# Optimization experiments

Measured on AMD Instinct MI355X. Metric: run time of the kernel, lower is better.

The kernel has to match this reference:

```python
import jax, jax.numpy as jnp
import numpy as np

HEADS = 4
ALPHA = 0.2  # leaky relu negative slope


def setup_inputs() -> dict:
    key = jax.random.key(0)
    ks = jax.random.split(key, 8)
    N, Fin, Fout = 4096, 512, 256
    return {
        "h": jax.random.normal(ks[0], (N, Fin), dtype=jnp.float32),
        "adj": jax.random.randint(ks[1], (N, N), 0, 2, dtype=jnp.int32),
        "W": jax.random.normal(ks[2], (Fin, Fout), dtype=jnp.float32) * (Fin ** -0.5),
        "Wl_w": jax.random.normal(ks[3], (Fout, Fout), dtype=jnp.float32) * (Fout ** -0.5),
        "Wl_b": jax.random.normal(ks[4], (Fout,), dtype=jnp.float32) * 0.02,
        "Wqkv_w": jax.random.normal(ks[5], (3 * Fout, Fout), dtype=jnp.float32) * (Fout ** -0.5),
        "Wqkv_b": jax.random.normal(ks[6], (3 * Fout,), dtype=jnp.float32) * 0.02,
        "a": jax.random.normal(ks[7], (2 * Fout, 1), dtype=jnp.float32) * (Fout ** -0.5),
    }


def reference(h, adj, W, Wl_w, Wl_b, Wqkv_w, Wqkv_b, a):
    N = h.shape[0]
    Fout = W.shape[1]
    d = Fout // HEADS
    scale = Fout ** -0.5  # note: original scales by out_features^-0.5, not head_dim

    Wh = h @ W                      # [N, Fout]
    Wh = Wh @ Wl_w.T + Wl_b         # to_linear

    qkv = Wh @ Wqkv_w.T + Wqkv_b    # [N, 3*Fout]
    q, k, v = jnp.split(qkv, 3, axis=-1)
    to_heads = lambda t: t.reshape(N, HEADS, d).transpose(1, 0, 2)  # [H, N, d]
    q, k, v = to_heads(q), to_heads(k), to_heads(v)

    dots = jax.nn.softmax(jnp.einsum('hid,hjd->hij', q, k) * scale, axis=-1)  # [H,N,N]
    Wh0 = jnp.einsum('hij,hjd->hid', dots, v)            # [H, N, d]
    Wh0 = Wh0.transpose(1, 0, 2).reshape(N, Fout)        # i (h d)
    Wh0 = jax.nn.softmax(Wh0, axis=-1)

    # GAT score decomposed: e_ij = leakyrelu(Wh_i . a1 + Wh_j . a2)
    a1 = a[:Fout, 0]
    a2 = a[Fout:, 0]
    e = jax.nn.leaky_relu((Wh @ a1)[:, None] + (Wh @ a2)[None, :], negative_slope=ALPHA)

    dsum = dots.sum(axis=0)                              # [N, N]
    neg = jnp.float32(-9e15)
    attention = jnp.where(adj > 0, e + dsum, neg)
    attention = jax.nn.softmax(attention, axis=1)
    # dropout p=0.0 / eval mode -> identity

    h_prime = attention @ Wh + Wh0
    return jax.nn.elu(h_prime)  # concat=True
```

## Files before the change

### kernel.cpp

```cpp
#include <hip/hip_runtime.h>

typedef float  f32x4 __attribute__((ext_vector_type(4)));
typedef short  s16x8 __attribute__((ext_vector_type(8)));
typedef unsigned short u16x8 __attribute__((ext_vector_type(8)));

#define NROWS 4096
#define FOUT  256
#define ALPHA_LR 0.2f
#define SCALE 0.0625f
#define NEGV  -9.0e15f

static __device__ __forceinline__ unsigned short bf16_rne(float x) {
    unsigned u = __float_as_uint(x);
    u += 0x7fffu + ((u >> 16) & 1u);
    return (unsigned short)(u >> 16);
}
static __device__ __forceinline__ float bf2f(unsigned short h) {
    return __uint_as_float(((unsigned)h) << 16);
}
static __device__ __forceinline__ float wmax16(float v) {
#pragma unroll
    for (int o = 8; o; o >>= 1) v = fmaxf(v, __shfl_xor(v, o, 16));
    return v;
}
static __device__ __forceinline__ float wsum16(float v) {
#pragma unroll
    for (int o = 8; o; o >>= 1) v += __shfl_xor(v, o, 16);
    return v;
}
static __device__ __forceinline__ float wmax32(float v) {
#pragma unroll
    for (int o = 16; o; o >>= 1) v = fmaxf(v, __shfl_xor(v, o, 32));
    return v;
}
static __device__ __forceinline__ float wsum32(float v) {
#pragma unroll
    for (int o = 16; o; o >>= 1) v += __shfl_xor(v, o, 32);
    return v;
}

template <bool BT, bool BIAS, int EPI>
__global__ __launch_bounds__(256) void gemm_f32(
    const float* __restrict__ A, const float* __restrict__ B,
    const float* __restrict__ bias, float* __restrict__ C,
    unsigned short* __restrict__ o0, unsigned short* __restrict__ o1,
    unsigned short* __restrict__ o2,
    int M, int Nn, int K)
{
    __shared__ float As[16][68];
    __shared__ float Bs[16][68];

    const int tid = threadIdx.x;
    const int bm = blockIdx.y * 64;
    const int bn = blockIdx.x * 64;
    const int tx = tid & 15;
    const int ty = tid >> 4;

    float acc[4][4];
#pragma unroll
    for (int r = 0; r < 4; ++r)
#pragma unroll
        for (int c = 0; c < 4; ++c) acc[r][c] = 0.0f;

    for (int k0 = 0; k0 < K; k0 += 16) {
        __syncthreads();
        {
            const int r = tid >> 2;
            const int c4 = (tid & 3) * 4;
            float4 a4 = *(const float4*)&A[(size_t)(bm + r) * K + k0 + c4];
            As[c4 + 0][r] = a4.x; As[c4 + 1][r] = a4.y;
            As[c4 + 2][r] = a4.z; As[c4 + 3][r] = a4.w;
        }
        if (!BT) {
            const int r = tid >> 4;
            const int c4 = (tid & 15) * 4;
            *(float4*)&Bs[r][c4] = *(const float4*)&B[(size_t)(k0 + r) * Nn + bn + c4];
        } else {
            const int r = tid >> 2;
            const int c4 = (tid & 3) * 4;
            float4 b4 = *(const float4*)&B[(size_t)(bn + r) * K + k0 + c4];
            Bs[c4 + 0][r] = b4.x; Bs[c4 + 1][r] = b4.y;
            Bs[c4 + 2][r] = b4.z; Bs[c4 + 3][r] = b4.w;
        }
        __syncthreads();
#pragma unroll
        for (int kk = 0; kk < 16; ++kk) {
            float4 a4 = *(const float4*)&As[kk][ty * 4];
            float4 b4 = *(const float4*)&Bs[kk][tx * 4];
            acc[0][0] += a4.x * b4.x; acc[0][1] += a4.x * b4.y; acc[0][2] += a4.x * b4.z; acc[0][3] += a4.x * b4.w;
            acc[1][0] += a4.y * b4.x; acc[1][1] += a4.y * b4.y; acc[1][2] += a4.y * b4.z; acc[1][3] += a4.y * b4.w;
            acc[2][0] += a4.z * b4.x; acc[2][1] += a4.z * b4.y; acc[2][2] += a4.z * b4.z; acc[2][3] += a4.z * b4.w;
            acc[3][0] += a4.w * b4.x; acc[3][1] += a4.w * b4.y; acc[3][2] += a4.w * b4.z; acc[3][3] += a4.w * b4.w;
        }
    }

    float bv[4] = {0.f, 0.f, 0.f, 0.f};
    if (BIAS) {
#pragma unroll
        for (int c = 0; c < 4; ++c) bv[c] = bias[bn + tx * 4 + c];
    }

    if (EPI == 0) {
#pragma unroll
        for (int r = 0; r < 4; ++r) {
            float4 o;
            o.x = acc[r][0] + bv[0]; o.y = acc[r][1] + bv[1];
            o.z = acc[r][2] + bv[2]; o.w = acc[r][3] + bv[3];
            *(float4*)&C[(size_t)(bm + ty * 4 + r) * Nn + bn + tx * 4] = o;
        }
    } else {
#pragma unroll
        for (int r = 0; r < 4; ++r) {
            const int row = bm + ty * 4 + r;
#pragma unroll
            for (int c = 0; c < 4; ++c) {
                const int col = bn + tx * 4 + c;
                float v = acc[r][c] + bv[c];
                if (EPI == 1) {
                    C[(size_t)row * Nn + col] = v;
                    o0[(size_t)col * NROWS + row] = bf16_rne(v);
                } else {
                    if (col < 256)      o0[(size_t)row * 256 + col] = bf16_rne(v);
                    else if (col < 512) o1[(size_t)row * 256 + (col - 256)] = bf16_rne(v);
                    else                o2[(size_t)(col - 512) * NROWS + row] = bf16_rne(v);
                }
            }
        }
    }
}

__global__ __launch_bounds__(256) void compute_p(
    const float* __restrict__ Wh, const float* __restrict__ a,
    float* __restrict__ p1, float* __restrict__ p2)
{
    const int row = blockIdx.x * 16 + (threadIdx.x >> 4);
    const int c = threadIdx.x & 15;
    float s1 = 0.f, s2 = 0.f;
    for (int f = c; f < FOUT; f += 16) {
        float w = Wh[(size_t)row * FOUT + f];
        s1 += w * a[f];
        s2 += w * a[FOUT + f];
    }
    s1 = wsum16(s1);
    s2 = wsum16(s2);
    if (c == 0) { p1[row] = s1; p2[row] = s2; }
}

__global__ __launch_bounds__(256) void stats_kernel(
    const unsigned short* __restrict__ qh_g, const unsigned short* __restrict__ kh_g,
    float* __restrict__ stats)
{
    const int tid = threadIdx.x;
    const int h = tid >> 6;
    const int ln = tid & 63;
    const int l15 = ln & 15;
    const int lhi = ln >> 4;
    const int rt = blockIdx.x >> 3;
    const int ch = blockIdx.x & 7;
    const int i0 = rt * 16;

    s16x8 qA[2];
#pragma unroll
    for (int ks = 0; ks < 2; ++ks)
        qA[ks] = *(const s16x8*)(qh_g + (size_t)(i0 + l15) * 256 + h * 64 + ks * 32 + lhi * 8);

    float m[4], z[4];
#pragma unroll
    for (int r = 0; r < 4; ++r) { m[r] = -3.0e38f; z[r] = 0.f; }

    for (int tt = 0; tt < 16; ++tt) {
        const int j0 = ch * 512 + tt * 32;
        f32x4 acc[2] = {{0.f,0.f,0.f,0.f},{0.f,0.f,0.f,0.f}};
#pragma unroll
        for (int ks = 0; ks < 2; ++ks)
#pragma unroll
            for (int nt = 0; nt < 2; ++nt) {
                s16x8 kB = *(const s16x8*)(kh_g + (size_t)(j0 + nt * 16 + l15) * 256 +
                                           h * 64 + ks * 32 + lhi * 8);
                acc[nt] = __builtin_amdgcn_mfma_f32_16x16x32_bf16(qA[ks], kB, acc[nt], 0, 0, 0);
            }
#pragma unroll
        for (int r = 0; r < 4; ++r) {
            float s0 = acc[0][r] * SCALE, s1 = acc[1][r] * SCALE;
            float mn = fmaxf(m[r], fmaxf(s0, s1));
            z[r] = z[r] * __expf(m[r] - mn) + __expf(s0 - mn) + __expf(s1 - mn);
            m[r] = mn;
        }
    }
#pragma unroll
    for (int r = 0; r < 4; ++r) {
        float mm = m[r], zz = z[r];
#pragma unroll
        for (int o = 1; o < 16; o <<= 1) {
            float mo = __shfl_xor(mm, o, 16);
            float zo = __shfl_xor(zz, o, 16);
            float mn = fmaxf(mm, mo);
            zz = zz * __expf(mm - mn) + zo * __expf(mo - mn);
            mm = mn;
        }
        if (l15 == 0) {
            size_t idx = (((size_t)(i0 + lhi * 4 + r) * 4 + h) * 8 + ch) * 2;
            stats[idx] = mm;
            stats[idx + 1] = zz;
        }
    }
}

__global__ __launch_bounds__(512, 4) void main_attn(
    const unsigned short* __restrict__ qh_g, const unsigned short* __restrict__ kh_g,
    const unsigned short* __restrict__ vth_g, const unsigned short* __restrict__ wht_g,
    const float* __restrict__ stats, const float* __restrict__ p1g,
    const float* __restrict__ p2g, const int* __restrict__ adj,
    unsigned short* __restrict__ pacc_o, unsigned short* __restrict__ wacc_o,
    float* __restrict__ ml_o)
{
    enum { KT = 0, VT = 16896, WHT = 37376, DOTS = 57856, PTIL = 62976,
           ALP = 64256, MIZ = 64320, SMEMSZ = 64832 };
    __shared__ __align__(16) char smem[SMEMSZ];

    const int tid = threadIdx.x;
    const int w = tid >> 6;
    const int h = w & 3;
    const int jg = w >> 2;
    const int ln = tid & 63;
    const int l15 = ln & 15;
    const int lhi = ln >> 4;
    const int rt = blockIdx.x >> 1;
    const int ch = blockIdx.x & 1;
    const int i0 = rt * 16;
    const int jbase = ch * 2048;
    const int srow = tid >> 5;
    const int scol = tid & 31;

    if (tid < 64) {
        int hh = tid >> 4, row = tid & 15;
        const float* sb = stats + ((size_t)(i0 + row) * 4 + hh) * 16;
        float M = -3.0e38f, Z = 0.f;
#pragma unroll
        for (int c = 0; c < 8; ++c) {
            float mc = sb[c * 2], zc = sb[c * 2 + 1];
            float mn = fmaxf(M, mc);
            Z = Z * __expf(M - mn) + zc * __expf(mc - mn);
            M = mn;
        }
        ((float*)(smem + MIZ))[(hh * 16 + row) * 2] = M;
        ((float*)(smem + MIZ))[(hh * 16 + row) * 2 + 1] = 1.0f / Z;
    }

    int laK[2], gK[2], laV[2], gV[2];
#pragma unroll
    for (int it = 0; it < 2; ++it) {
        int c = tid + it * 512;
        int kr = c >> 5, kc = c & 31;
        laK[it] = kr * 528 + kc * 16;
        gK[it] = kr * 256 + kc * 8;
        int vd = c >> 2, vc = c & 3;
        laV[it] = vd * 80 + vc * 16;
        gV[it] = vd * 4096 + vc * 8;
    }

#pragma unroll
    for (int it = 0; it < 2; ++it) {
        *(uint4*)(smem + KT + laK[it])  = *(const uint4*)(kh_g  + (size_t)jbase * 256 + gK[it]);
        *(uint4*)(smem + VT + laV[it])  = *(const uint4*)(vth_g + (size_t)jbase + gV[it]);
        *(uint4*)(smem + WHT + laV[it]) = *(const uint4*)(wht_g + (size_t)jbase + gV[it]);
    }

    s16x8 qA[2];
#pragma unroll
    for (int ks = 0; ks < 2; ++ks)
        qA[ks] = *(const s16x8*)(qh_g + (size_t)(i0 + l15) * 256 + h * 64 + ks * 32 + lhi * 8);

    __syncthreads();

    float m_f[4], iz_f[4];
#pragma unroll
    for (int r = 0; r < 4; ++r) {
        m_f[r]  = ((float*)(smem + MIZ))[(h * 16 + lhi * 4 + r) * 2];
        iz_f[r] = ((float*)(smem + MIZ))[(h * 16 + lhi * 4 + r) * 2 + 1];
    }

    int kaddr[2];
#pragma unroll
    for (int ks = 0; ks < 2; ++ks)
        kaddr[ks] = KT + (jg * 16 + l15) * 528 + h * 128 + ks * 64 + lhi * 16;
    const int daddr = DOTS + h * 1280 + l15 * 80 + lhi * 16;
    const int paddr = PTIL + l15 * 80 + lhi * 16;
    int vaddr[2], waddr[2];
#pragma unroll
    for (int nt = 0; nt < 2; ++nt) {
        int d = h * 64 + jg * 32 + nt * 16 + l15;
        vaddr[nt] = VT + d * 80 + lhi * 16;
        waddr[nt] = WHT + d * 80 + lhi * 16;
    }
    const int dwbase = DOTS + h * 1280 + jg * 32 + l15 * 2;

    f32x4 pacc[2] = {{0.f,0.f,0.f,0.f},{0.f,0.f,0.f,0.f}};
    f32x4 wacc[2] = {{0.f,0.f,0.f,0.f},{0.f,0.f,0.f,0.f}};
    float Mrun = -3.0e38f, Lrun = 0.0f;
    const float p1v = p1g[i0 + srow];

    int   adjc = adj[(size_t)(i0 + srow) * NROWS + jbase + scol];
    float p2c  = p2g[jbase + scol];

    for (int t = 0; t < 64; ++t) {
        const int jn = jbase + ((t + 1) & 63) * 32;
        uint4 kr0 = *(const uint4*)(kh_g + (size_t)jn * 256 + gK[0]);
        uint4 kr1 = *(const uint4*)(kh_g + (size_t)jn * 256 + gK[1]);

        f32x4 qk = {0.f,0.f,0.f,0.f};
        __builtin_amdgcn_s_setprio(1);
        {
            s16x8 k0 = *(const s16x8*)(smem + kaddr[0]);
            s16x8 k1 = *(const s16x8*)(smem + kaddr[1]);
            qk = __builtin_amdgcn_mfma_f32_16x16x32_bf16(qA[0], k0, qk, 0, 0, 0);
            qk = __builtin_amdgcn_mfma_f32_16x16x32_bf16(qA[1], k1, qk, 0, 0, 0);
        }
        __builtin_amdgcn_s_setprio(0);
#pragma unroll
        for (int r = 0; r < 4; ++r) {
            float d = __expf(qk[r] * SCALE - m_f[r]) * iz_f[r];
            *(unsigned short*)(smem + dwbase + (lhi * 4 + r) * 80) = bf16_rne(d);
        }
        __syncthreads();

        *(uint4*)(smem + KT + laK[0]) = kr0;
        *(uint4*)(smem + KT + laK[1]) = kr1;
        uint4 vr0 = *(const uint4*)(vth_g + (size_t)jn + gV[0]);
        uint4 vr1 = *(const uint4*)(vth_g + (size_t)jn + gV[1]);
        uint4 wr0 = *(const uint4*)(wht_g + (size_t)jn + gV[0]);
        uint4 wr1 = *(const uint4*)(wht_g + (size_t)jn + gV[1]);
        int   adjn = adj[(size_t)(i0 + srow) * NROWS + jn + scol];
        float p2n  = p2g[jn + scol];

        __builtin_amdgcn_s_setprio(1);
        {
            s16x8 dA = *(const s16x8*)(smem + daddr);
            s16x8 v0 = *(const s16x8*)(smem + vaddr[0]);
            s16x8 v1 = *(const s16x8*)(smem + vaddr[1]);
            pacc[0] = __builtin_amdgcn_mfma_f32_16x16x32_bf16(dA, v0, pacc[0], 0, 0, 0);
            pacc[1] = __builtin_amdgcn_mfma_f32_16x16x32_bf16(dA, v1, pacc[1], 0, 0, 0);
        }
        __builtin_amdgcn_s_setprio(0);

        {
            float ds = 0.f;
#pragma unroll
            for (int hh = 0; hh < 4; ++hh)
                ds += bf2f(*(const unsigned short*)(smem + DOTS + hh * 1280 + srow * 80 + scol * 2));
            float e = p1v + p2c; e = e > 0.f ? e : ALPHA_LR * e;
            float l = adjc > 0 ? e + ds : NEGV;
            float tm = wmax32(l);
            float Mn = fmaxf(Mrun, tm);
            float p = __expf(l - Mn);
            float ps = wsum32(p);
            float al = __expf(Mrun - Mn);
            Lrun = Lrun * al + ps;
            Mrun = Mn;
            if ((ln & 31) == 0) *(float*)(smem + ALP + srow * 4) = al;
            *(unsigned short*)(smem + PTIL + srow * 80 + scol * 2) = bf16_rne(p);
        }
        __syncthreads();

        *(uint4*)(smem + VT + laV[0]) = vr0;
        *(uint4*)(smem + VT + laV[1]) = vr1;

        {
            float al_r[4];
#pragma unroll
            for (int r = 0; r < 4; ++r)
                al_r[r] = *(const float*)(smem + ALP + (lhi * 4 + r) * 4);
#pragma unroll
            for (int nt = 0; nt < 2; ++nt)
#pragma unroll
                for (int r = 0; r < 4; ++r) wacc[nt][r] *= al_r[r];
            s16x8 pA = *(const s16x8*)(smem + paddr);
            s16x8 w0 = *(const s16x8*)(smem + waddr[0]);
            s16x8 w1 = *(const s16x8*)(smem + waddr[1]);
            __builtin_amdgcn_s_setprio(1);
            wacc[0] = __builtin_amdgcn_mfma_f32_16x16x32_bf16(pA, w0, wacc[0], 0, 0, 0);
            wacc[1] = __builtin_amdgcn_mfma_f32_16x16x32_bf16(pA, w1, wacc[1], 0, 0, 0);
            __builtin_amdgcn_s_setprio(0);
        }
        __syncthreads();

        *(uint4*)(smem + WHT + laV[0]) = wr0;
        *(uint4*)(smem + WHT + laV[1]) = wr1;

        adjc = adjn; p2c = p2n;
    }

    const size_t pbase = (size_t)(rt * 2 + ch) * 16 * 256;
#pragma unroll
    for (int nt = 0; nt < 2; ++nt)
#pragma unroll
        for (int r = 0; r < 4; ++r) {
            int row = lhi * 4 + r;
            int col = h * 64 + jg * 32 + nt * 16 + l15;
            pacc_o[pbase + row * 256 + col] = bf16_rne(pacc[nt][r]);
            wacc_o[pbase + row * 256 + col] = bf16_rne(wacc[nt][r]);
        }
    if ((ln & 31) == 0) {
        ml_o[((size_t)(rt * 2 + ch) * 16 + srow) * 2]     = Mrun;
        ml_o[((size_t)(rt * 2 + ch) * 16 + srow) * 2 + 1] = Lrun;
    }
}

__global__ __launch_bounds__(256) void merge_kernel(
    const unsigned short* __restrict__ pacc_b, const unsigned short* __restrict__ wacc_b,
    const float* __restrict__ ml, float* __restrict__ out)
{
    const int rt = blockIdx.x;
    const int tid = threadIdx.x;
    const int row = tid >> 4;
    const int cg = tid & 15;

    const size_t b0 = ((size_t)(rt * 2 + 0) * 16 + row) * 256 + cg * 16;
    const size_t b1 = ((size_t)(rt * 2 + 1) * 16 + row) * 256 + cg * 16;
    float M0 = ml[((size_t)(rt * 2 + 0) * 16 + row) * 2];
    float L0 = ml[((size_t)(rt * 2 + 0) * 16 + row) * 2 + 1];
    float M1 = ml[((size_t)(rt * 2 + 1) * 16 + row) * 2];
    float L1 = ml[((size_t)(rt * 2 + 1) * 16 + row) * 2 + 1];
    float M = fmaxf(M0, M1);
    float s0 = __expf(M0 - M), s1 = __expf(M1 - M);
    float invL = 1.0f / (L0 * s0 + L1 * s1);

    u16x8 pa[2][2], wa[2][2];
#pragma unroll
    for (int k = 0; k < 2; ++k) {
        pa[0][k] = *(const u16x8*)(pacc_b + b0 + k * 8);
        pa[1][k] = *(const u16x8*)(pacc_b + b1 + k * 8);
        wa[0][k] = *(const u16x8*)(wacc_b + b0 + k * 8);
        wa[1][k] = *(const u16x8*)(wacc_b + b1 + k * 8);
    }
    float p[16], wv[16];
    float mx = -3.0e38f;
#pragma unroll
    for (int k = 0; k < 16; ++k) {
        p[k] = bf2f(pa[0][k >> 3][k & 7]) + bf2f(pa[1][k >> 3][k & 7]);
        wv[k] = (bf2f(wa[0][k >> 3][k & 7]) * s0 + bf2f(wa[1][k >> 3][k & 7]) * s1) * invL;
        mx = fmaxf(mx, p[k]);
    }
    mx = wmax16(mx);
    float sm = 0.f;
#pragma unroll
    for (int k = 0; k < 16; ++k) { p[k] = __expf(p[k] - mx); sm += p[k]; }
    sm = wsum16(sm);
    float inv = 1.0f / sm;
    float* orow = out + ((size_t)(rt * 16 + row)) * 256 + cg * 16;
#pragma unroll
    for (int k4 = 0; k4 < 4; ++k4) {
        float4 o;
        float v;
        v = wv[k4*4+0] + p[k4*4+0] * inv; o.x = v > 0.f ? v : __expf(v) - 1.f;
        v = wv[k4*4+1] + p[k4*4+1] * inv; o.y = v > 0.f ? v : __expf(v) - 1.f;
        v = wv[k4*4+2] + p[k4*4+2] * inv; o.z = v > 0.f ? v : __expf(v) - 1.f;
        v = wv[k4*4+3] + p[k4*4+3] * inv; o.w = v > 0.f ? v : __expf(v) - 1.f;
        *(float4*)(orow + k4 * 4) = o;
    }
}

extern "C" void kernel_launch(void* const* d_in, const int* in_sizes, int n_in,
                              void* d_out, int out_size, void* d_ws, size_t ws_size,
                              hipStream_t stream)
{
    const float* h      = (const float*)d_in[0];
    const int*   adj    = (const int*)d_in[1];
    const float* W      = (const float*)d_in[2];
    const float* Wl_w   = (const float*)d_in[3];
    const float* Wl_b   = (const float*)d_in[4];
    const float* Wqkv_w = (const float*)d_in[5];
    const float* Wqkv_b = (const float*)d_in[6];
    const float* a      = (const float*)d_in[7];
    float* out = (float*)d_out;

    float* ws = (float*)d_ws;
    float* T   = ws;
    float* Whb = ws + (1 << 20);
    unsigned short* qh  = (unsigned short*)(ws + (2 << 20));
    unsigned short* kh  = qh + (1 << 20);
    unsigned short* vth = kh + (1 << 20);
    unsigned short* wht = vth + (1 << 20);
    float* p1b    = ws + (4 << 20);
    float* p2b    = p1b + 4096;
    float* statsb = p2b + 4096;
    float* mlb    = statsb + 262144;
    unsigned short* pacc_b = (unsigned short*)T;
    unsigned short* wacc_b = (unsigned short*)Whb;

    dim3 blk(256);
    gemm_f32<false, false, 0><<<dim3(4, 64), blk, 0, stream>>>(
        h, W, nullptr, T, nullptr, nullptr, nullptr, 4096, 256, 512);
    gemm_f32<true, true, 1><<<dim3(4, 64), blk, 0, stream>>>(
        T, Wl_w, Wl_b, Whb, wht, nullptr, nullptr, 4096, 256, 256);
    gemm_f32<true, true, 2><<<dim3(12, 64), blk, 0, stream>>>(
        Whb, Wqkv_w, Wqkv_b, nullptr, qh, kh, vth, 4096, 768, 256);
    compute_p<<<dim3(256), blk, 0, stream>>>(Whb, a, p1b, p2b);
    stats_kernel<<<dim3(2048), blk, 0, stream>>>(qh, kh, statsb);
    main_attn<<<dim3(512), dim3(512), 0, stream>>>(
        qh, kh, vth, wht, statsb, p1b, p2b, adj, pacc_b, wacc_b, mlb);
    merge_kernel<<<dim3(256), blk, 0, stream>>>(pacc_b, wacc_b, mlb, out);
}
```

Before: 289.6 us.

## Use split-bf16 MFMA GEMMs, fold W into Wl, and stream attention operands from registers

Replaces the FP32 SIMT GEMMs with MFMA GEMMs that emulate fp32 precision by splitting each operand into bf16 hi/lo parts and issuing three MFMAs per tile. The two input linear layers are algebraically combined: Wl_w·Wᵀ is computed once into a combined weight, so the large 4096-row pass runs a single GEMM instead of two. Separately, main_attn drops its K/V/Wh LDS staging and instead loads MFMA fragments straight from global memory into registers with one-step prefetch, cutting shared memory and one barrier per iteration. The trade-offs are slightly different rounding from the hi/lo split and reassociated GEMMs, plus less coalesced global fragment loads in the attention loop.

```diff
diff --git a/kernel.cpp b/kernel.cpp
--- a/kernel.cpp
+++ b/kernel.cpp
@@ -15,6 +15,9 @@
     u += 0x7fffu + ((u >> 16) & 1u);
     return (unsigned short)(u >> 16);
 }
+static __device__ __forceinline__ unsigned short bf16_trunc(float x) {
+    return (unsigned short)(__float_as_uint(x) >> 16);
+}
 static __device__ __forceinline__ float bf2f(unsigned short h) {
     return __uint_as_float(((unsigned)h) << 16);
 }
@@ -39,91 +42,117 @@
     return v;
 }
 
-template <bool BT, bool BIAS, int EPI>
-__global__ __launch_bounds__(256) void gemm_f32(
-    const float* __restrict__ A, const float* __restrict__ B,
-    const float* __restrict__ bias, float* __restrict__ C,
-    unsigned short* __restrict__ o0, unsigned short* __restrict__ o1,
-    unsigned short* __restrict__ o2,
+__global__ __launch_bounds__(256) void wprep(
+    const float* __restrict__ W, const float* __restrict__ Wq,
+    unsigned short* __restrict__ Whi, unsigned short* __restrict__ Wlo,
+    unsigned short* __restrict__ Qhi, unsigned short* __restrict__ Qlo)
+{
+    int i = blockIdx.x * 256 + threadIdx.x;
+    if (i < 131072) {
+        float v = W[i];
+        unsigned short hh = bf16_trunc(v);
+        Whi[i] = hh; Wlo[i] = bf16_rne(v - bf2f(hh));
+    }
+    if (i < 196608) {
+        float v = Wq[i];
+        unsigned short hh = bf16_trunc(v);
+        Qhi[i] = hh; Qlo[i] = bf16_rne(v - bf2f(hh));
+    }
+}
+
+template <int EPI, bool BIAS>
+__global__ __launch_bounds__(256) void gemm_mfma(
+    const float* __restrict__ A,
+    const unsigned short* __restrict__ Bhi, const unsigned short* __restrict__ Blo,
+    const float* __restrict__ bias,
+    float* __restrict__ C, unsigned short* __restrict__ o0,
+    unsigned short* __restrict__ o1, unsigned short* __restrict__ o2,
     int M, int Nn, int K)
 {
-    __shared__ float As[16][68];
-    __shared__ float Bs[16][68];
+    __shared__ unsigned short Ah[64][40];
+    __shared__ unsigned short Al[64][40];
+    __shared__ unsigned short Bh[64][40];
+    __shared__ unsigned short Bl[64][40];
 
     const int tid = threadIdx.x;
+    const int w = tid >> 6;
+    const int ln = tid & 63;
+    const int l15 = ln & 15;
+    const int lhi = ln >> 4;
     const int bm = blockIdx.y * 64;
     const int bn = blockIdx.x * 64;
-    const int tx = tid & 15;
-    const int ty = tid >> 4;
-
-    float acc[4][4];
-#pragma unroll
-    for (int r = 0; r < 4; ++r)
-#pragma unroll
-        for (int c = 0; c < 4; ++c) acc[r][c] = 0.0f;
-
-    for (int k0 = 0; k0 < K; k0 += 16) {
+    const int sm = tid >> 2;
+    const int sk = (tid & 3) * 8;
+
+    f32x4 acc[4];
+#pragma unroll
+    for (int cf = 0; cf < 4; ++cf) acc[cf] = (f32x4){0.f, 0.f, 0.f, 0.f};
+
+    const float* arow = &A[(size_t)(bm + sm) * K];
+    const unsigned short* bhrow = &Bhi[(size_t)(bn + sm) * K];
+    const unsigned short* blrow = &Blo[(size_t)(bn + sm) * K];
+
+    float4 a0r = *(const float4*)(arow + sk);
+    float4 a1r = *(const float4*)(arow + sk + 4);
+    uint4 bhr = *(const uint4*)(bhrow + sk);
+    uint4 blr = *(const uint4*)(blrow + sk);
+
+    for (int k0 = 0; k0 < K; k0 += 32) {
+        float vv[8] = {a0r.x, a0r.y, a0r.z, a0r.w, a1r.x, a1r.y, a1r.z, a1r.w};
+        unsigned hp[4], lp[4];
+#pragma unroll
+        for (int q = 0; q < 4; ++q) {
+            unsigned short h0 = bf16_trunc(vv[q * 2]);
+            unsigned short h1 = bf16_trunc(vv[q * 2 + 1]);
+            unsigned short l0 = bf16_rne(vv[q * 2] - bf2f(h0));
+            unsigned short l1 = bf16_rne(vv[q * 2 + 1] - bf2f(h1));
+            hp[q] = (unsigned)h0 | ((unsigned)h1 << 16);
+            lp[q] = (unsigned)l0 | ((unsigned)l1 << 16);
+        }
         __syncthreads();
-        {
-            const int r = tid >> 2;
-            const int c4 = (tid & 3) * 4;
-            float4 a4 = *(const float4*)&A[(size_t)(bm + r) * K + k0 + c4];
-            As[c4 + 0][r] = a4.x; As[c4 + 1][r] = a4.y;
-            As[c4 + 2][r] = a4.z; As[c4 + 3][r] = a4.w;
-        }
-        if (!BT) {
-            const int r = tid >> 4;
-            const int c4 = (tid & 15) * 4;
-            *(float4*)&Bs[r][c4] = *(const float4*)&B[(size_t)(k0 + r) * Nn + bn + c4];
-        } else {
-            const int r = tid >> 2;
-            const int c4 = (tid & 3) * 4;
-            float4 b4 = *(const float4*)&B[(size_t)(bn + r) * K + k0 + c4];
-            Bs[c4 + 0][r] = b4.x; Bs[c4 + 1][r] = b4.y;
-            Bs[c4 + 2][r] = b4.z; Bs[c4 + 3][r] = b4.w;
-        }
+        *(uint4*)&Ah[sm][sk] = make_uint4(hp[0], hp[1], hp[2], hp[3]);
+        *(uint4*)&Al[sm][sk] = make_uint4(lp[0], lp[1], lp[2], lp[3]);
+        *(uint4*)&Bh[sm][sk] = bhr;
+        *(uint4*)&Bl[sm][sk] = blr;
+        const int kn = (k0 + 32 < K) ? k0 + 32 : 0;
+        a0r = *(const float4*)(arow + kn + sk);
+        a1r = *(const float4*)(arow + kn + sk + 4);
+        bhr = *(const uint4*)(bhrow + kn + sk);
+        blr = *(const uint4*)(blrow + kn + sk);
         __syncthreads();
-#pragma unroll
-        for (int kk = 0; kk < 16; ++kk) {
-            float4 a4 = *(const float4*)&As[kk][ty * 4];
-            float4 b4 = *(const float4*)&Bs[kk][tx * 4];
-            acc[0][0] += a4.x * b4.x; acc[0][1] += a4.x * b4.y; acc[0][2] += a4.x * b4.z; acc[0][3] += a4.x * b4.w;
-            acc[1][0] += a4.y * b4.x; acc[1][1] += a4.y * b4.y; acc[1][2] += a4.y * b4.z; acc[1][3] += a4.y * b4.w;
-            acc[2][0] += a4.z * b4.x; acc[2][1] += a4.z * b4.y; acc[2][2] += a4.z * b4.z; acc[2][3] += a4.z * b4.w;
-            acc[3][0] += a4.w * b4.x; acc[3][1] += a4.w * b4.y; acc[3][2] += a4.w * b4.z; acc[3][3] += a4.w * b4.w;
-        }
-    }
-
-    float bv[4] = {0.f, 0.f, 0.f, 0.f};
-    if (BIAS) {
-#pragma unroll
-        for (int c = 0; c < 4; ++c) bv[c] = bias[bn + tx * 4 + c];
-    }
-
-    if (EPI == 0) {
+        s16x8 ah = *(const s16x8*)&Ah[w * 16 + l15][lhi * 8];
+        s16x8 al2 = *(const s16x8*)&Al[w * 16 + l15][lhi * 8];
+        __builtin_amdgcn_s_setprio(1);
+#pragma unroll
+        for (int cf = 0; cf < 4; ++cf) {
+            s16x8 bh = *(const s16x8*)&Bh[cf * 16 + l15][lhi * 8];
+            s16x8 bl = *(const s16x8*)&Bl[cf * 16 + l15][lhi * 8];
+            acc[cf] = __builtin_amdgcn_mfma_f32_16x16x32_bf16(ah, bh, acc[cf], 0, 0, 0);
+            acc[cf] = __builtin_amdgcn_mfma_f32_16x16x32_bf16(ah, bl, acc[cf], 0, 0, 0);
+            acc[cf] = __builtin_amdgcn_mfma_f32_16x16x32_bf16(al2, bh, acc[cf], 0, 0, 0);
+        }
+        __builtin_amdgcn_s_setprio(0);
+    }
+
+#pragma unroll
+    for (int cf = 0; cf < 4; ++cf) {
+        const int col = bn + cf * 16 + l15;
+        float bv = BIAS ? bias[col] : 0.0f;
 #pragma unroll
         for (int r = 0; r < 4; ++r) {
-            float4 o;
-            o.x = acc[r][0] + bv[0]; o.y = acc[r][1] + bv[1];
-            o.z = acc[r][2] + bv[2]; o.w = acc[r][3] + bv[3];
-            *(float4*)&C[(size_t)(bm + ty * 4 + r) * Nn + bn + tx * 4] = o;
-        }
-    } else {
-#pragma unroll
-        for (int r = 0; r < 4; ++r) {
-            const int row = bm + ty * 4 + r;
-#pragma unroll
-            for (int c = 0; c < 4; ++c) {
-                const int col = bn + tx * 4 + c;
-                float v = acc[r][c] + bv[c];
-                if (EPI == 1) {
-                    C[(size_t)row * Nn + col] = v;
-                    o0[(size_t)col * NROWS + row] = bf16_rne(v);
-                } else {
-                    if (col < 256)      o0[(size_t)row * 256 + col] = bf16_rne(v);
-                    else if (col < 512) o1[(size_t)row * 256 + (col - 256)] = bf16_rne(v);
-                    else                o2[(size_t)(col - 512) * NROWS + row] = bf16_rne(v);
-                }
+            const int row = bm + w * 16 + lhi * 4 + r;
+            float v = acc[cf][r] + bv;
+            if (EPI == 1) {
+                C[(size_t)row * Nn + col] = v;
+                o0[(size_t)col * NROWS + row] = bf16_rne(v);
+            } else if (EPI == 2) {
+                if (col < 256)      o0[(size_t)row * 256 + col] = bf16_rne(v);
+                else if (col < 512) o1[(size_t)row * 256 + (col - 256)] = bf16_rne(v);
+                else                o2[(size_t)(col - 512) * NROWS + row] = bf16_rne(v);
+            } else {
+                unsigned short hh = bf16_trunc(v);
+                o0[(size_t)row * Nn + col] = hh;
+                o1[(size_t)row * Nn + col] = bf16_rne(v - bf2f(hh));
             }
         }
     }
@@ -214,8 +243,7 @@
     unsigned short* __restrict__ pacc_o, unsigned short* __restrict__ wacc_o,
     float* __restrict__ ml_o)
 {
-    enum { KT = 0, VT = 16896, WHT = 37376, DOTS = 57856, PTIL = 62976,
-           ALP = 64256, MIZ = 64320, SMEMSZ = 64832 };
+    enum { DOTS = 0, PTIL = 5120, ALP = 6400, MIZ = 6464, SMEMSZ = 6976 };
     __shared__ __align__(16) char smem[SMEMSZ];
 
     const int tid = threadIdx.x;
@@ -247,25 +275,6 @@
         ((float*)(smem + MIZ))[(hh * 16 + row) * 2 + 1] = 1.0f / Z;
     }
 
-    int laK[2], gK[2], laV[2], gV[2];
-#pragma unroll
-    for (int it = 0; it < 2; ++it) {
-        int c = tid + it * 512;
-        int kr = c >> 5, kc = c & 31;
-        laK[it] = kr * 528 + kc * 16;
-        gK[it] = kr * 256 + kc * 8;
-        int vd = c >> 2, vc = c & 3;
-        laV[it] = vd * 80 + vc * 16;
-        gV[it] = vd * 4096 + vc * 8;
-    }
-
-#pragma unroll
-    for (int it = 0; it < 2; ++it) {
-        *(uint4*)(smem + KT + laK[it])  = *(const uint4*)(kh_g  + (size_t)jbase * 256 + gK[it]);
-        *(uint4*)(smem + VT + laV[it])  = *(const uint4*)(vth_g + (size_t)jbase + gV[it]);
-        *(uint4*)(smem + WHT + laV[it]) = *(const uint4*)(wht_g + (size_t)jbase + gV[it]);
-    }
-
     s16x8 qA[2];
 #pragma unroll
     for (int ks = 0; ks < 2; ++ks)
@@ -280,43 +289,38 @@
         iz_f[r] = ((float*)(smem + MIZ))[(h * 16 + lhi * 4 + r) * 2 + 1];
     }
 
-    int kaddr[2];
-#pragma unroll
-    for (int ks = 0; ks < 2; ++ks)
-        kaddr[ks] = KT + (jg * 16 + l15) * 528 + h * 128 + ks * 64 + lhi * 16;
-    const int daddr = DOTS + h * 1280 + l15 * 80 + lhi * 16;
-    const int paddr = PTIL + l15 * 80 + lhi * 16;
-    int vaddr[2], waddr[2];
-#pragma unroll
-    for (int nt = 0; nt < 2; ++nt) {
-        int d = h * 64 + jg * 32 + nt * 16 + l15;
-        vaddr[nt] = VT + d * 80 + lhi * 16;
-        waddr[nt] = WHT + d * 80 + lhi * 16;
-    }
-    const int dwbase = DOTS + h * 1280 + jg * 32 + l15 * 2;
+    const unsigned short* kp = kh_g + (size_t)(jg * 16 + l15) * 256 + h * 64 + lhi * 8;
+    const unsigned short* vp = vth_g + (size_t)(h * 64 + jg * 32 + l15) * 4096 + lhi * 8;
+    const unsigned short* wp = wht_g + (size_t)(h * 64 + jg * 32 + l15) * 4096 + lhi * 8;
+
+    s16x8 kf0 = *(const s16x8*)(kp + (size_t)jbase * 256);
+    s16x8 kf1 = *(const s16x8*)(kp + (size_t)jbase * 256 + 32);
+    s16x8 vf0 = *(const s16x8*)(vp + jbase);
+    s16x8 vf1 = *(const s16x8*)(vp + 16 * 4096 + jbase);
+    s16x8 wf0 = *(const s16x8*)(wp + jbase);
+    s16x8 wf1 = *(const s16x8*)(wp + 16 * 4096 + jbase);
+    int   adjc = adj[(size_t)(i0 + srow) * NROWS + jbase + scol];
+    float p2c  = p2g[jbase + scol];
 
     f32x4 pacc[2] = {{0.f,0.f,0.f,0.f},{0.f,0.f,0.f,0.f}};
     f32x4 wacc[2] = {{0.f,0.f,0.f,0.f},{0.f,0.f,0.f,0.f}};
     float Mrun = -3.0e38f, Lrun = 0.0f;
     const float p1v = p1g[i0 + srow];
 
-    int   adjc = adj[(size_t)(i0 + srow) * NROWS + jbase + scol];
-    float p2c  = p2g[jbase + scol];
+    const int dwbase = DOTS + h * 1280 + (jg * 16 + l15) * 2;
+    const int daddr  = DOTS + h * 1280 + l15 * 80 + lhi * 16;
+    const int paddr  = PTIL + l15 * 80 + lhi * 16;
 
     for (int t = 0; t < 64; ++t) {
         const int jn = jbase + ((t + 1) & 63) * 32;
-        uint4 kr0 = *(const uint4*)(kh_g + (size_t)jn * 256 + gK[0]);
-        uint4 kr1 = *(const uint4*)(kh_g + (size_t)jn * 256 + gK[1]);
-
-        f32x4 qk = {0.f,0.f,0.f,0.f};
+
+        f32x4 qk = {0.f, 0.f, 0.f, 0.f};
         __builtin_amdgcn_s_setprio(1);
-        {
-            s16x8 k0 = *(const s16x8*)(smem + kaddr[0]);
-            s16x8 k1 = *(const s16x8*)(smem + kaddr[1]);
-            qk = __builtin_amdgcn_mfma_f32_16x16x32_bf16(qA[0], k0, qk, 0, 0, 0);
-            qk = __builtin_amdgcn_mfma_f32_16x16x32_bf16(qA[1], k1, qk, 0, 0, 0);
-        }
+        qk = __builtin_amdgcn_mfma_f32_16x16x32_bf16(qA[0], kf0, qk, 0, 0, 0);
+        qk = __builtin_amdgcn_mfma_f32_16x16x32_bf16(qA[1], kf1, qk, 0, 0, 0);
         __builtin_amdgcn_s_setprio(0);
+        kf0 = *(const s16x8*)(kp + (size_t)jn * 256);
+        kf1 = *(const s16x8*)(kp + (size_t)jn * 256 + 32);
 #pragma unroll
         for (int r = 0; r < 4; ++r) {
             float d = __expf(qk[r] * SCALE - m_f[r]) * iz_f[r];
@@ -324,24 +328,15 @@
         }
         __syncthreads();
 
-        *(uint4*)(smem + KT + laK[0]) = kr0;
-        *(uint4*)(smem + KT + laK[1]) = kr1;
-        uint4 vr0 = *(const uint4*)(vth_g + (size_t)jn + gV[0]);
-        uint4 vr1 = *(const uint4*)(vth_g + (size_t)jn + gV[1]);
-        uint4 wr0 = *(const uint4*)(wht_g + (size_t)jn + gV[0]);
-        uint4 wr1 = *(const uint4*)(wht_g + (size_t)jn + gV[1]);
-        int   adjn = adj[(size_t)(i0 + srow) * NROWS + jn + scol];
-        float p2n  = p2g[jn + scol];
-
-        __builtin_amdgcn_s_setprio(1);
         {
             s16x8 dA = *(const s16x8*)(smem + daddr);
-            s16x8 v0 = *(const s16x8*)(smem + vaddr[0]);
-            s16x8 v1 = *(const s16x8*)(smem + vaddr[1]);
-            pacc[0] = __builtin_amdgcn_mfma_f32_16x16x32_bf16(dA, v0, pacc[0], 0, 0, 0);
-            pacc[1] = __builtin_amdgcn_mfma_f32_16x16x32_bf16(dA, v1, pacc[1], 0, 0, 0);
-        }
-        __builtin_amdgcn_s_setprio(0);
+            __builtin_amdgcn_s_setprio(1);
+            pacc[0] = __builtin_amdgcn_mfma_f32_16x16x32_bf16(dA, vf0, pacc[0], 0, 0, 0);
+            pacc[1] = __builtin_amdgcn_mfma_f32_16x16x32_bf16(dA, vf1, pacc[1], 0, 0, 0);
+            __builtin_amdgcn_s_setprio(0);
+        }
+        vf0 = *(const s16x8*)(vp + jn);
+        vf1 = *(const s16x8*)(vp + 16 * 4096 + jn);
 
         {
             float ds = 0.f;
@@ -360,34 +355,27 @@
             if ((ln & 31) == 0) *(float*)(smem + ALP + srow * 4) = al;
             *(unsigned short*)(smem + PTIL + srow * 80 + scol * 2) = bf16_rne(p);
         }
+        adjc = adj[(size_t)(i0 + srow) * NROWS + jn + scol];
+        p2c  = p2g[jn + scol];
         __syncthreads();
 
-        *(uint4*)(smem + VT + laV[0]) = vr0;
-        *(uint4*)(smem + VT + laV[1]) = vr1;
-
         {
-            float al_r[4];
+            float alr[4];
 #pragma unroll
             for (int r = 0; r < 4; ++r)
-                al_r[r] = *(const float*)(smem + ALP + (lhi * 4 + r) * 4);
+                alr[r] = *(const float*)(smem + ALP + (lhi * 4 + r) * 4);
 #pragma unroll
             for (int nt = 0; nt < 2; ++nt)
 #pragma unroll
-                for (int r = 0; r < 4; ++r) wacc[nt][r] *= al_r[r];
+                for (int r = 0; r < 4; ++r) wacc[nt][r] *= alr[r];
             s16x8 pA = *(const s16x8*)(smem + paddr);
-            s16x8 w0 = *(const s16x8*)(smem + waddr[0]);
-            s16x8 w1 = *(const s16x8*)(smem + waddr[1]);
             __builtin_amdgcn_s_setprio(1);
-            wacc[0] = __builtin_amdgcn_mfma_f32_16x16x32_bf16(pA, w0, wacc[0], 0, 0, 0);
-            wacc[1] = __builtin_amdgcn_mfma_f32_16x16x32_bf16(pA, w1, wacc[1], 0, 0, 0);
+            wacc[0] = __builtin_amdgcn_mfma_f32_16x16x32_bf16(pA, wf0, wacc[0], 0, 0, 0);
+            wacc[1] = __builtin_amdgcn_mfma_f32_16x16x32_bf16(pA, wf1, wacc[1], 0, 0, 0);
             __builtin_amdgcn_s_setprio(0);
         }
-        __syncthreads();
-
-        *(uint4*)(smem + WHT + laV[0]) = wr0;
-        *(uint4*)(smem + WHT + laV[1]) = wr1;
-
-        adjc = adjn; p2c = p2n;
+        wf0 = *(const s16x8*)(wp + jn);
+        wf1 = *(const s16x8*)(wp + 16 * 4096 + jn);
     }
 
     const size_t pbase = (size_t)(rt * 2 + ch) * 16 * 256;
@@ -475,26 +463,33 @@
     float* out = (float*)d_out;
 
     float* ws = (float*)d_ws;
-    float* T   = ws;
-    float* Whb = ws + (1 << 20);
-    unsigned short* qh  = (unsigned short*)(ws + (2 << 20));
-    unsigned short* kh  = qh + (1 << 20);
-    unsigned short* vth = kh + (1 << 20);
-    unsigned short* wht = vth + (1 << 20);
-    float* p1b    = ws + (4 << 20);
+    float* Whb = ws;
+    unsigned short* u16b  = (unsigned short*)(ws + (1 << 20));
+    unsigned short* qh    = u16b;
+    unsigned short* kh    = u16b + (1 << 20);
+    unsigned short* vth   = u16b + (2 << 20);
+    unsigned short* wht   = u16b + (3 << 20);
+    unsigned short* Whi   = u16b + (4 << 20);
+    unsigned short* Wlo   = Whi + 131072;
+    unsigned short* Qhi   = Wlo + 131072;
+    unsigned short* Qlo   = Qhi + 196608;
+    unsigned short* WcThi = Qlo + 196608;
+    unsigned short* WcTlo = WcThi + 131072;
+    float* p1b    = ws + 3670016;
     float* p2b    = p1b + 4096;
     float* statsb = p2b + 4096;
     float* mlb    = statsb + 262144;
-    unsigned short* pacc_b = (unsigned short*)T;
-    unsigned short* wacc_b = (unsigned short*)Whb;
+    unsigned short* pacc_b = (unsigned short*)Whb;
+    unsigned short* wacc_b = (unsigned short*)(ws + 3960832);
 
     dim3 blk(256);
-    gemm_f32<false, false, 0><<<dim3(4, 64), blk, 0, stream>>>(
-        h, W, nullptr, T, nullptr, nullptr, nullptr, 4096, 256, 512);
-    gemm_f32<true, true, 1><<<dim3(4, 64), blk, 0, stream>>>(
-        T, Wl_w, Wl_b, Whb, wht, nullptr, nullptr, 4096, 256, 256);
-    gemm_f32<true, true, 2><<<dim3(12, 64), blk, 0, stream>>>(
-        Whb, Wqkv_w, Wqkv_b, nullptr, qh, kh, vth, 4096, 768, 256);
+    wprep<<<dim3(768), blk, 0, stream>>>(W, Wqkv_w, Whi, Wlo, Qhi, Qlo);
+    gemm_mfma<3, false><<<dim3(8, 4), blk, 0, stream>>>(
+        Wl_w, Whi, Wlo, nullptr, nullptr, WcThi, WcTlo, nullptr, 256, 512, 256);
+    gemm_mfma<1, true><<<dim3(4, 64), blk, 0, stream>>>(
+        h, WcThi, WcTlo, Wl_b, Whb, wht, nullptr, nullptr, 4096, 256, 512);
+    gemm_mfma<2, true><<<dim3(12, 64), blk, 0, stream>>>(
+        Whb, Qhi, Qlo, Wqkv_b, nullptr, qh, kh, vth, 4096, 768, 256);
     compute_p<<<dim3(256), blk, 0, stream>>>(Whb, a, p1b, p2b);
     stats_kernel<<<dim3(2048), blk, 0, stream>>>(qh, kh, statsb);
     main_attn<<<dim3(512), dim3(512), 0, stream>>>(
```

Measured after the change: 290.2 us. Within noise of the previous version (+0.2%).
